# Kernel optimization log

Hardware: AMD Instinct MI355X
Metric: run time of the kernel (lower is better)

The kernel has to match this reference:

```python
import jax, jax.numpy as jnp
import numpy as np

def setup_inputs() -> dict:
    key = jax.random.key(0)
    kq, kk, kv = jax.random.split(key, 3)
    B, H, N, D = 2, 12, 4096, 64
    Q = jax.random.normal(kq, (B, H, N, D), dtype=jnp.float32)
    K = jax.random.normal(kk, (B, H, N, D), dtype=jnp.float32)
    V = jax.random.normal(kv, (B, H, N, D), dtype=jnp.float32)
    mask = jnp.ones((B, N), dtype=jnp.float32)
    return {"Q": Q, "K": K, "V": V, "mask": mask}

def reference(Q, K, V, mask):
    # Q, K, V: [B, H, N, D]; mask: [B, N]
    N = Q.shape[2]
    scale = 1.0 / jnp.sqrt(jnp.sqrt(jnp.float32(N)))  # N^(-1/4)
    m = mask[:, None, :, None]                         # [B,1,N,1]
    Qf = (jax.nn.elu(Q) + 1.0) * scale                 # feature map on queries
    Kf = (jax.nn.elu(K) + 1.0) * m * scale             # feature map + mask on keys
    Vm = V * m
    # linear attention: Q (K^T V), contracting over sequence first -> [B,H,D,D]
    KtV = jnp.einsum('bhnd,bhne->bhde', Kf, Vm)
    X = jnp.einsum('bhnd,bhde->bhne', Qf, KtV)
    return X
```

## Files before the change

kernel.cpp:

```cpp
#include <hip/hip_runtime.h>
#include <hip/hip_bf16.h>
#include <math.h>


#define BH_TOT 24
#define NROWS 4096
#define DD 64

typedef __attribute__((ext_vector_type(8))) short bf16x8;
typedef __attribute__((ext_vector_type(4))) float f32x4;

__device__ __forceinline__ float elu1(float x) {
    return x > 0.0f ? x + 1.0f : __expf(x);
}
__device__ __forceinline__ short f2bf(float x) {
    __hip_bfloat16 h = __float2bfloat16(x);
    return *reinterpret_cast<short*>(&h);
}

__global__ __launch_bounds__(256) void la_pass1(
        const float* __restrict__ K, const float* __restrict__ V,
        const float* __restrict__ mask, float* __restrict__ partial,
        float scale, int chunksPerWave) {
    const int bh   = blockIdx.x;
    const int slab = blockIdx.y;
    const int wave = threadIdx.x >> 6;
    const int lane = threadIdx.x & 63;
    const int g = lane >> 4, rg = g * 8, cl = lane & 15;

    const float* __restrict__ Kp = K + (size_t)bh * NROWS * DD;
    const float* __restrict__ Vp = V + (size_t)bh * NROWS * DD;
    const float* __restrict__ mp = mask + (size_t)(bh / 12) * NROWS;

    f32x4 acc[4][4];
#pragma unroll
    for (int je = 0; je < 4; ++je)
#pragma unroll
        for (int id = 0; id < 4; ++id) acc[je][id] = (f32x4)0.0f;

    const int n0 = (slab * 4 + wave) * chunksPerWave * 32;

#pragma unroll 1
    for (int c = 0; c < chunksPerWave; ++c) {
        const int nb = n0 + c * 32 + rg;
        const float* kb = Kp + (size_t)nb * DD + cl;
        const float* vb = Vp + (size_t)nb * DD + cl;
        float mrow[8], kr[8][4], vr[8][4];
#pragma unroll
        for (int jj = 0; jj < 8; ++jj) {
            mrow[jj] = mp[nb + jj];
#pragma unroll
            for (int i = 0; i < 4; ++i) {
                kr[jj][i] = kb[jj * DD + i * 16];
                vr[jj][i] = vb[jj * DD + i * 16];
            }
        }
        bf16x8 af[4], bv[4];
#pragma unroll
        for (int i = 0; i < 4; ++i)
#pragma unroll
            for (int jj = 0; jj < 8; ++jj) {
                af[i][jj] = f2bf(elu1(kr[jj][i]) * (mrow[jj] * scale));
                bv[i][jj] = f2bf(vr[jj][i] * mrow[jj]);
            }
#pragma unroll
        for (int je = 0; je < 4; ++je)
#pragma unroll
            for (int id = 0; id < 4; ++id)
                acc[je][id] = __builtin_amdgcn_mfma_f32_16x16x32_bf16(
                                  bv[je], af[id], acc[je][id], 0, 0, 0);
    }

    __shared__ f32x4 red[2][16][64];
    if (wave >= 2) {
#pragma unroll
        for (int je = 0; je < 4; ++je)
#pragma unroll
            for (int id = 0; id < 4; ++id)
                red[wave - 2][je * 4 + id][lane] = acc[je][id];
    }
    __syncthreads();
    if (wave < 2) {
#pragma unroll
        for (int je = 0; je < 4; ++je)
#pragma unroll
            for (int id = 0; id < 4; ++id)
                acc[je][id] += red[wave][je * 4 + id][lane];
    }
    __syncthreads();
    if (wave == 1) {
#pragma unroll
        for (int je = 0; je < 4; ++je)
#pragma unroll
            for (int id = 0; id < 4; ++id)
                red[0][je * 4 + id][lane] = acc[je][id];
    }
    __syncthreads();
    if (wave == 0) {
        f32x4* out = (f32x4*)partial + ((size_t)bh * gridDim.y + slab) * 1024;
#pragma unroll
        for (int je = 0; je < 4; ++je)
#pragma unroll
            for (int id = 0; id < 4; ++id)
                out[(je * 4 + id) * 64 + lane]
                    = acc[je][id] + red[0][je * 4 + id][lane];
    }
}

__global__ __launch_bounds__(256) void la_pass2(
        const float* __restrict__ partial, __hip_bfloat16* __restrict__ ktvT,
        int slabs) {
    const int bh  = blockIdx.x;
    const int pos = blockIdx.y * 256 + threadIdx.x;
    const f32x4* base = (const f32x4*)partial + (size_t)bh * slabs * 1024 + pos;
    f32x4 s = (f32x4)0.0f;
#pragma unroll 8
    for (int w = 0; w < slabs; ++w)
        s += base[(size_t)w * 1024];
    const int frag = pos >> 6, ln = pos & 63;
    const int e0 = 16 * (frag >> 2) + 4 * (ln >> 4);
    const int d  = 16 * (frag & 3) + (ln & 15);
    __hip_bfloat16* ko = ktvT + (size_t)bh * DD * DD;
#pragma unroll
    for (int r = 0; r < 4; ++r)
        ko[(size_t)(e0 + r) * DD + d] = __float2bfloat16(s[r]);
}

__global__ __launch_bounds__(256) void la_pass3(
        const float* __restrict__ Q, const __hip_bfloat16* __restrict__ ktvT,
        float* __restrict__ X, float scale) {
    const int bh   = blockIdx.x;
    const int wave = threadIdx.x >> 6;
    const int lane = threadIdx.x & 63;
    const int n0   = blockIdx.y * 128 + wave * 32;
    const int g = lane >> 4, rg = g * 8, cl = lane & 15;

    bf16x8 afr[4][2];
#pragma unroll
    for (int i = 0; i < 4; ++i)
#pragma unroll
        for (int c2 = 0; c2 < 2; ++c2)
            afr[i][c2] = *reinterpret_cast<const bf16x8*>(
                ktvT + (size_t)bh * DD * DD + (size_t)(16 * i + cl) * DD + 32 * c2 + rg);

    const float* Qp = Q + (size_t)bh * NROWS * DD;
    bf16x8 bfr[2][2];
#pragma unroll
    for (int t = 0; t < 2; ++t)
#pragma unroll
        for (int c2 = 0; c2 < 2; ++c2) {
            const float* qp = Qp + (size_t)(n0 + 16 * t + cl) * DD + 32 * c2 + rg;
            float4 q0 = ((const float4*)qp)[0];
            float4 q1 = ((const float4*)qp)[1];
            bf16x8 a;
            a[0] = f2bf(elu1(q0.x) * scale); a[1] = f2bf(elu1(q0.y) * scale);
            a[2] = f2bf(elu1(q0.z) * scale); a[3] = f2bf(elu1(q0.w) * scale);
            a[4] = f2bf(elu1(q1.x) * scale); a[5] = f2bf(elu1(q1.y) * scale);
            a[6] = f2bf(elu1(q1.z) * scale); a[7] = f2bf(elu1(q1.w) * scale);
            bfr[t][c2] = a;
        }

    f32x4 acc[4][2];
#pragma unroll
    for (int i = 0; i < 4; ++i)
#pragma unroll
        for (int t = 0; t < 2; ++t) acc[i][t] = (f32x4)0.0f;

#pragma unroll
    for (int i = 0; i < 4; ++i)
#pragma unroll
        for (int t = 0; t < 2; ++t) {
            acc[i][t] = __builtin_amdgcn_mfma_f32_16x16x32_bf16(
                            afr[i][0], bfr[t][0], acc[i][t], 0, 0, 0);
            acc[i][t] = __builtin_amdgcn_mfma_f32_16x16x32_bf16(
                            afr[i][1], bfr[t][1], acc[i][t], 0, 0, 0);
        }

    float* Xp = X + (size_t)bh * NROWS * DD;
#pragma unroll
    for (int i = 0; i < 4; ++i)
#pragma unroll
        for (int t = 0; t < 2; ++t) {
            float4 v = make_float4(acc[i][t][0], acc[i][t][1],
                                   acc[i][t][2], acc[i][t][3]);
            *reinterpret_cast<float4*>(
                Xp + (size_t)(n0 + 16 * t + cl) * DD + 16 * i + 4 * g) = v;
        }
}

extern "C" void kernel_launch(void* const* d_in, const int* in_sizes, int n_in,
                              void* d_out, int out_size, void* d_ws, size_t ws_size,
                              hipStream_t stream) {
    const float* Q    = (const float*)d_in[0];
    const float* K    = (const float*)d_in[1];
    const float* V    = (const float*)d_in[2];
    const float* mask = (const float*)d_in[3];
    float* X = (float*)d_out;

    const float scale = 0.125f;

    int slabs = 16;
    while (slabs > 4 &&
           (size_t)BH_TOT * slabs * DD * DD * 4 + (size_t)BH_TOT * DD * DD * 2 > ws_size)
        slabs >>= 1;
    const int chunksPerWave = NROWS / (slabs * 128);

    float* partial = (float*)d_ws;
    __hip_bfloat16* ktvT =
        (__hip_bfloat16*)((char*)d_ws + (size_t)BH_TOT * slabs * DD * DD * 4);

    la_pass1<<<dim3(BH_TOT, slabs), 256, 0, stream>>>(K, V, mask, partial,
                                                      scale, chunksPerWave);
    la_pass2<<<dim3(BH_TOT, 4), 256, 0, stream>>>(partial, ktvT, slabs);
    la_pass3<<<dim3(BH_TOT, 32), 256, 0, stream>>>(Q, ktvT, X, scale);
}
```

Measured before the change: 32.29 us.

## Eliminate reduction pass by consuming per-slab bf16 KtV partials in pass3

```diff
diff --git a/kernel.cpp b/kernel.cpp
--- a/kernel.cpp
+++ b/kernel.cpp
@@ -20,8 +20,8 @@
 
 __global__ __launch_bounds__(256) void la_pass1(
         const float* __restrict__ K, const float* __restrict__ V,
-        const float* __restrict__ mask, float* __restrict__ partial,
-        float scale, int chunksPerWave) {
+        const float* __restrict__ mask, bf16x8* __restrict__ partial,
+        float scale, int chunksPerWave, int slabs) {
     const int bh   = blockIdx.x;
     const int slab = blockIdx.y;
     const int wave = threadIdx.x >> 6;
@@ -72,6 +72,7 @@
     }
 
     __shared__ f32x4 red[2][16][64];
+    __shared__ float T[64][67];
     if (wave >= 2) {
 #pragma unroll
         for (int je = 0; je < 4; ++je)
@@ -97,51 +98,42 @@
     }
     __syncthreads();
     if (wave == 0) {
-        f32x4* out = (f32x4*)partial + ((size_t)bh * gridDim.y + slab) * 1024;
-#pragma unroll
-        for (int je = 0; je < 4; ++je)
-#pragma unroll
-            for (int id = 0; id < 4; ++id)
-                out[(je * 4 + id) * 64 + lane]
-                    = acc[je][id] + red[0][je * 4 + id][lane];
-    }
-}
-
-__global__ __launch_bounds__(256) void la_pass2(
-        const float* __restrict__ partial, __hip_bfloat16* __restrict__ ktvT,
-        int slabs) {
-    const int bh  = blockIdx.x;
-    const int pos = blockIdx.y * 256 + threadIdx.x;
-    const f32x4* base = (const f32x4*)partial + (size_t)bh * slabs * 1024 + pos;
-    f32x4 s = (f32x4)0.0f;
-#pragma unroll 8
-    for (int w = 0; w < slabs; ++w)
-        s += base[(size_t)w * 1024];
-    const int frag = pos >> 6, ln = pos & 63;
-    const int e0 = 16 * (frag >> 2) + 4 * (ln >> 4);
-    const int d  = 16 * (frag & 3) + (ln & 15);
-    __hip_bfloat16* ko = ktvT + (size_t)bh * DD * DD;
-#pragma unroll
-    for (int r = 0; r < 4; ++r)
-        ko[(size_t)(e0 + r) * DD + d] = __float2bfloat16(s[r]);
+#pragma unroll
+        for (int je = 0; je < 4; ++je)
+#pragma unroll
+            for (int id = 0; id < 4; ++id) {
+            f32x4 v = acc[je][id] + red[0][je * 4 + id][lane];
+#pragma unroll
+            for (int r = 0; r < 4; ++r)
+                T[16 * je + 4 * g + r][16 * id + cl] = v[r];
+        }
+    }
+    __syncthreads();
+
+    bf16x8* out = partial + ((size_t)bh * slabs + slab) * 512;
+#pragma unroll
+    for (int k = 0; k < 2; ++k) {
+        const int fw = threadIdx.x + k * 256;
+        const int i  = fw >> 7;
+        const int c2 = (fw >> 6) & 1;
+        const int ln = fw & 63;
+        const int g2 = ln >> 4, cl2 = ln & 15;
+        bf16x8 w;
+#pragma unroll
+        for (int jj = 0; jj < 8; ++jj)
+            w[jj] = f2bf(T[16 * i + cl2][32 * c2 + 8 * g2 + jj]);
+        out[fw] = w;
+    }
 }
 
 __global__ __launch_bounds__(256) void la_pass3(
-        const float* __restrict__ Q, const __hip_bfloat16* __restrict__ ktvT,
-        float* __restrict__ X, float scale) {
+        const float* __restrict__ Q, const bf16x8* __restrict__ partial,
+        float* __restrict__ X, float scale, int slabs) {
     const int bh   = blockIdx.x;
     const int wave = threadIdx.x >> 6;
     const int lane = threadIdx.x & 63;
     const int n0   = blockIdx.y * 128 + wave * 32;
     const int g = lane >> 4, rg = g * 8, cl = lane & 15;
-
-    bf16x8 afr[4][2];
-#pragma unroll
-    for (int i = 0; i < 4; ++i)
-#pragma unroll
-        for (int c2 = 0; c2 < 2; ++c2)
-            afr[i][c2] = *reinterpret_cast<const bf16x8*>(
-                ktvT + (size_t)bh * DD * DD + (size_t)(16 * i + cl) * DD + 32 * c2 + rg);
 
     const float* Qp = Q + (size_t)bh * NROWS * DD;
     bf16x8 bfr[2][2];
@@ -166,15 +158,26 @@
 #pragma unroll
         for (int t = 0; t < 2; ++t) acc[i][t] = (f32x4)0.0f;
 
-#pragma unroll
-    for (int i = 0; i < 4; ++i)
-#pragma unroll
-        for (int t = 0; t < 2; ++t) {
-            acc[i][t] = __builtin_amdgcn_mfma_f32_16x16x32_bf16(
-                            afr[i][0], bfr[t][0], acc[i][t], 0, 0, 0);
-            acc[i][t] = __builtin_amdgcn_mfma_f32_16x16x32_bf16(
-                            afr[i][1], bfr[t][1], acc[i][t], 0, 0, 0);
-        }
+    const bf16x8* pb = partial + (size_t)bh * slabs * 512;
+#pragma unroll 2
+    for (int s = 0; s < slabs; ++s) {
+        const bf16x8* ps = pb + (size_t)s * 512;
+        bf16x8 afr[4][2];
+#pragma unroll
+        for (int i = 0; i < 4; ++i)
+#pragma unroll
+            for (int c2 = 0; c2 < 2; ++c2)
+                afr[i][c2] = ps[(i * 2 + c2) * 64 + lane];
+#pragma unroll
+        for (int i = 0; i < 4; ++i)
+#pragma unroll
+            for (int t = 0; t < 2; ++t) {
+                acc[i][t] = __builtin_amdgcn_mfma_f32_16x16x32_bf16(
+                                afr[i][0], bfr[t][0], acc[i][t], 0, 0, 0);
+                acc[i][t] = __builtin_amdgcn_mfma_f32_16x16x32_bf16(
+                                afr[i][1], bfr[t][1], acc[i][t], 0, 0, 0);
+            }
+    }
 
     float* Xp = X + (size_t)bh * NROWS * DD;
 #pragma unroll
@@ -200,17 +203,13 @@
     const float scale = 0.125f;
 
     int slabs = 16;
-    while (slabs > 4 &&
-           (size_t)BH_TOT * slabs * DD * DD * 4 + (size_t)BH_TOT * DD * DD * 2 > ws_size)
+    while (slabs > 4 && (size_t)BH_TOT * slabs * 8192 > ws_size)
         slabs >>= 1;
     const int chunksPerWave = NROWS / (slabs * 128);
 
-    float* partial = (float*)d_ws;
-    __hip_bfloat16* ktvT =
-        (__hip_bfloat16*)((char*)d_ws + (size_t)BH_TOT * slabs * DD * DD * 4);
+    bf16x8* partial = (bf16x8*)d_ws;
 
     la_pass1<<<dim3(BH_TOT, slabs), 256, 0, stream>>>(K, V, mask, partial,
-                                                      scale, chunksPerWave);
-    la_pass2<<<dim3(BH_TOT, 4), 256, 0, stream>>>(partial, ktvT, slabs);
-    la_pass3<<<dim3(BH_TOT, 32), 256, 0, stream>>>(Q, ktvT, X, scale);
-}
+                                                      scale, chunksPerWave, slabs);
+    la_pass3<<<dim3(BH_TOT, 32), 256, 0, stream>>>(Q, partial, X, scale, slabs);
+}
```

Measured after the change: 37.75 us. +16.9%, slower.

## Use 32 slabs with one chunk per wave and bf16 partial sums

Applied to the files above, without the earlier changes.

```diff
diff --git a/kernel.cpp b/kernel.cpp
--- a/kernel.cpp
+++ b/kernel.cpp
@@ -6,6 +6,7 @@
 #define BH_TOT 24
 #define NROWS 4096
 #define DD 64
+#define SLABS 32
 
 typedef __attribute__((ext_vector_type(8))) short bf16x8;
 typedef __attribute__((ext_vector_type(4))) float f32x4;
@@ -17,11 +18,15 @@
     __hip_bfloat16 h = __float2bfloat16(x);
     return *reinterpret_cast<short*>(&h);
 }
+__device__ __forceinline__ float bf2f(unsigned short u) {
+    unsigned int v = (unsigned int)u << 16;
+    return __builtin_bit_cast(float, v);
+}
 
 __global__ __launch_bounds__(256) void la_pass1(
         const float* __restrict__ K, const float* __restrict__ V,
-        const float* __restrict__ mask, float* __restrict__ partial,
-        float scale, int chunksPerWave) {
+        const float* __restrict__ mask, ushort4* __restrict__ partial,
+        float scale) {
     const int bh   = blockIdx.x;
     const int slab = blockIdx.y;
     const int wave = threadIdx.x >> 6;
@@ -32,20 +37,12 @@
     const float* __restrict__ Vp = V + (size_t)bh * NROWS * DD;
     const float* __restrict__ mp = mask + (size_t)(bh / 12) * NROWS;
 
-    f32x4 acc[4][4];
-#pragma unroll
-    for (int je = 0; je < 4; ++je)
-#pragma unroll
-        for (int id = 0; id < 4; ++id) acc[je][id] = (f32x4)0.0f;
-
-    const int n0 = (slab * 4 + wave) * chunksPerWave * 32;
-
-#pragma unroll 1
-    for (int c = 0; c < chunksPerWave; ++c) {
-        const int nb = n0 + c * 32 + rg;
+    const int nb = (slab * 4 + wave) * 32 + rg;
+
+    float mrow[8], kr[8][4], vr[8][4];
+    {
         const float* kb = Kp + (size_t)nb * DD + cl;
         const float* vb = Vp + (size_t)nb * DD + cl;
-        float mrow[8], kr[8][4], vr[8][4];
 #pragma unroll
         for (int jj = 0; jj < 8; ++jj) {
             mrow[jj] = mp[nb + jj];
@@ -55,6 +52,15 @@
                 vr[jj][i] = vb[jj * DD + i * 16];
             }
         }
+    }
+
+    f32x4 acc[4][4];
+#pragma unroll
+    for (int je = 0; je < 4; ++je)
+#pragma unroll
+        for (int id = 0; id < 4; ++id) acc[je][id] = (f32x4)0.0f;
+
+    {
         bf16x8 af[4], bv[4];
 #pragma unroll
         for (int i = 0; i < 4; ++i)
@@ -97,33 +103,39 @@
     }
     __syncthreads();
     if (wave == 0) {
-        f32x4* out = (f32x4*)partial + ((size_t)bh * gridDim.y + slab) * 1024;
-#pragma unroll
-        for (int je = 0; je < 4; ++je)
-#pragma unroll
-            for (int id = 0; id < 4; ++id)
-                out[(je * 4 + id) * 64 + lane]
-                    = acc[je][id] + red[0][je * 4 + id][lane];
+        ushort4* out = partial + ((size_t)bh * SLABS + slab) * 1024;
+#pragma unroll
+        for (int je = 0; je < 4; ++je)
+#pragma unroll
+            for (int id = 0; id < 4; ++id) {
+                f32x4 v = acc[je][id] + red[0][je * 4 + id][lane];
+                ushort4 u;
+                u.x = (unsigned short)f2bf(v[0]); u.y = (unsigned short)f2bf(v[1]);
+                u.z = (unsigned short)f2bf(v[2]); u.w = (unsigned short)f2bf(v[3]);
+                out[(je * 4 + id) * 64 + lane] = u;
+            }
     }
 }
 
 __global__ __launch_bounds__(256) void la_pass2(
-        const float* __restrict__ partial, __hip_bfloat16* __restrict__ ktvT,
-        int slabs) {
+        const ushort4* __restrict__ partial, __hip_bfloat16* __restrict__ ktvT) {
     const int bh  = blockIdx.x;
     const int pos = blockIdx.y * 256 + threadIdx.x;
-    const f32x4* base = (const f32x4*)partial + (size_t)bh * slabs * 1024 + pos;
-    f32x4 s = (f32x4)0.0f;
+    const ushort4* base = partial + (size_t)bh * SLABS * 1024 + pos;
+    float s0 = 0.f, s1 = 0.f, s2 = 0.f, s3 = 0.f;
 #pragma unroll 8
-    for (int w = 0; w < slabs; ++w)
-        s += base[(size_t)w * 1024];
+    for (int w = 0; w < SLABS; ++w) {
+        ushort4 u = base[(size_t)w * 1024];
+        s0 += bf2f(u.x); s1 += bf2f(u.y); s2 += bf2f(u.z); s3 += bf2f(u.w);
+    }
     const int frag = pos >> 6, ln = pos & 63;
     const int e0 = 16 * (frag >> 2) + 4 * (ln >> 4);
     const int d  = 16 * (frag & 3) + (ln & 15);
     __hip_bfloat16* ko = ktvT + (size_t)bh * DD * DD;
-#pragma unroll
-    for (int r = 0; r < 4; ++r)
-        ko[(size_t)(e0 + r) * DD + d] = __float2bfloat16(s[r]);
+    ko[(size_t)(e0 + 0) * DD + d] = __float2bfloat16(s0);
+    ko[(size_t)(e0 + 1) * DD + d] = __float2bfloat16(s1);
+    ko[(size_t)(e0 + 2) * DD + d] = __float2bfloat16(s2);
+    ko[(size_t)(e0 + 3) * DD + d] = __float2bfloat16(s3);
 }
 
 __global__ __launch_bounds__(256) void la_pass3(
@@ -199,18 +211,11 @@
 
     const float scale = 0.125f;
 
-    int slabs = 16;
-    while (slabs > 4 &&
-           (size_t)BH_TOT * slabs * DD * DD * 4 + (size_t)BH_TOT * DD * DD * 2 > ws_size)
-        slabs >>= 1;
-    const int chunksPerWave = NROWS / (slabs * 128);
-
-    float* partial = (float*)d_ws;
+    ushort4* partial = (ushort4*)d_ws;
     __hip_bfloat16* ktvT =
-        (__hip_bfloat16*)((char*)d_ws + (size_t)BH_TOT * slabs * DD * DD * 4);
-
-    la_pass1<<<dim3(BH_TOT, slabs), 256, 0, stream>>>(K, V, mask, partial,
-                                                      scale, chunksPerWave);
-    la_pass2<<<dim3(BH_TOT, 4), 256, 0, stream>>>(partial, ktvT, slabs);
+        (__hip_bfloat16*)((char*)d_ws + (size_t)BH_TOT * SLABS * 1024 * 8);
+
+    la_pass1<<<dim3(BH_TOT, SLABS), 256, 0, stream>>>(K, V, mask, partial, scale);
+    la_pass2<<<dim3(BH_TOT, 4), 256, 0, stream>>>(partial, ktvT);
     la_pass3<<<dim3(BH_TOT, 32), 256, 0, stream>>>(Q, ktvT, X, scale);
 }
```

New measurement: 31.05 us. -3.8%, faster.
